# Optimization experiments

Hardware: AMD Instinct MI355X
Metric: run time of the kernel (lower is better)

The kernel has to match this reference:

```python
import jax, jax.numpy as jnp
import numpy as np

CHANNEL = 64
RATIO = 8
C1 = CHANNEL // RATIO


def setup_inputs() -> dict:
    key = jax.random.key(0)
    ks = jax.random.split(key, 8)
    b, c, h, w = 2, CHANNEL, 96, 96
    X = jax.random.normal(ks[0], (b, c, h, w), dtype=jnp.float32)
    Y = jax.random.normal(ks[1], (b, c, h, w), dtype=jnp.float32)
    # 1x1 conv weights (stored as [out, in]) + biases, Kaiming-ish scale
    s = 1.0 / np.sqrt(c)
    Wq = jax.random.uniform(ks[2], (C1, c), jnp.float32, -s, s)
    bq = jax.random.uniform(ks[3], (C1,), jnp.float32, -s, s)
    Wk = jax.random.uniform(ks[4], (C1, c), jnp.float32, -s, s)
    bk = jax.random.uniform(ks[5], (C1,), jnp.float32, -s, s)
    Wv = jax.random.uniform(ks[6], (c, c), jnp.float32, -s, s)
    bv = jax.random.uniform(ks[7], (c,), jnp.float32, -s, s)
    return {"X": X, "Y": Y, "Wq": Wq, "bq": bq, "Wk": Wk, "bk": bk, "Wv": Wv, "bv": bv}


def reference(X, Y, Wq, bq, Wk, bk, Wv, bv):
    b, c, h, w = Y.shape
    n = h * w
    # 1x1 convs as channel contractions -> [b, n, c_out]
    Xf = X.reshape(b, c, n)                       # [b, c, n]
    q = jnp.einsum('oc,bcn->bno', Wq, Xf) + bq    # [b, n, c1]
    k = jnp.einsum('oc,bcn->bno', Wk, Xf) + bk    # [b, n, c1]
    v = jnp.einsum('oc,bcn->bno', Wv, Y.reshape(b, c, n)) + bv  # [b, n, c]
    scores = jnp.einsum('bic,bjc->bij', q, k)     # [b, n, n]
    # NOTE: softmax over dim=1 (the first n axis), as in the original module
    a = jax.nn.softmax(scores, axis=1)
    x = jnp.einsum('bij,bjc->bic', a, v)          # [b, n, c]
    x = x.transpose(0, 2, 1).reshape(b, c, h, w)
    return Y + x
```

## Files before the change

### kernel.cpp

```cpp
#include <hip/hip_runtime.h>

#define NPOS 9216
#define NB 2
#define CCH 64

typedef __attribute__((ext_vector_type(8))) short short8;
typedef __attribute__((ext_vector_type(4))) float f32x4;

__device__ __forceinline__ ushort f2bf(float x) {
    unsigned u = __builtin_bit_cast(unsigned, x);
    u += 0x7FFFu + ((u >> 16) & 1u);
    return (ushort)(u >> 16);
}

__global__ __launch_bounds__(256) void qkv_kernel(
    const float* __restrict__ X, const float* __restrict__ Y,
    const float* __restrict__ Wq, const float* __restrict__ bq,
    const float* __restrict__ Wk, const float* __restrict__ bk,
    const float* __restrict__ Wv, const float* __restrict__ bv,
    ushort* __restrict__ qb, ushort* __restrict__ kb, float* __restrict__ v)
{
    __shared__ float wqkT[1024];
    __shared__ float wvT[4096];
    int tid = threadIdx.x;
    for (int idx = tid; idx < 1024; idx += 256) {
        int c = idx >> 4, o = idx & 15;
        wqkT[idx] = (o < 8) ? Wq[o * 64 + c] : Wk[(o - 8) * 64 + c];
    }
    for (int idx = tid; idx < 4096; idx += 256) {
        int c = idx >> 6, o = idx & 63;
        wvT[idx] = Wv[o * 64 + c];
    }
    __syncthreads();

    int p = tid & 63, s = tid >> 6;
    int base = blockIdx.x * 64;
    int b = base / NPOS;
    int n = (base % NPOS) + p;

    float va[16], qk[8];
    #pragma unroll
    for (int o = 0; o < 16; ++o) va[o] = bv[s * 16 + o];
    #pragma unroll
    for (int o = 0; o < 8; ++o) qk[o] = 0.f;
    if (s == 0) {
        #pragma unroll
        for (int o = 0; o < 8; ++o) qk[o] = bq[o];
    } else if (s == 1) {
        #pragma unroll
        for (int o = 0; o < 8; ++o) qk[o] = bk[o];
    }

    const float* Xb = X + (size_t)b * CCH * NPOS + n;
    const float* Yb = Y + (size_t)b * CCH * NPOS + n;
    for (int c = 0; c < 64; ++c) {
        float yv = Yb[(size_t)c * NPOS];
        const float4* wv4 = (const float4*)(wvT + c * 64 + s * 16);
        #pragma unroll
        for (int o4 = 0; o4 < 4; ++o4) {
            float4 wv = wv4[o4];
            va[o4*4+0] += wv.x * yv; va[o4*4+1] += wv.y * yv;
            va[o4*4+2] += wv.z * yv; va[o4*4+3] += wv.w * yv;
        }
        if (s < 2) {
            float xv = Xb[(size_t)c * NPOS];
            const float4* wq4 = (const float4*)(wqkT + c * 16 + s * 8);
            float4 w0 = wq4[0], w1 = wq4[1];
            qk[0] += w0.x * xv; qk[1] += w0.y * xv;
            qk[2] += w0.z * xv; qk[3] += w0.w * xv;
            qk[4] += w1.x * xv; qk[5] += w1.y * xv;
            qk[6] += w1.z * xv; qk[7] += w1.w * xv;
        }
    }
    float4* vdst = (float4*)(v + ((size_t)b * NPOS + n) * 64 + s * 16);
    #pragma unroll
    for (int o4 = 0; o4 < 4; ++o4)
        vdst[o4] = make_float4(va[o4*4], va[o4*4+1], va[o4*4+2], va[o4*4+3]);
    if (s < 2) {
        short8 row;
        #pragma unroll
        for (int o = 0; o < 8; ++o) row[o] = (short)f2bf(qk[o]);
        ushort* dst = (s == 0 ? qb : kb) + ((size_t)b * NPOS + n) * 8;
        *(short8*)dst = row;
    }
}

__global__ __launch_bounds__(256) void zpass_kernel(
    const ushort* __restrict__ qb, const ushort* __restrict__ kb,
    float* __restrict__ Z)
{
    int tid = threadIdx.x;
    int w = tid >> 6, l = tid & 63;
    int il = l & 15, g = l >> 4;
    int b = blockIdx.z;
    int jb = blockIdx.x * 64 + w * 16;
    const short8 zero8 = {0,0,0,0,0,0,0,0};
    const f32x4 cz = {0.f,0.f,0.f,0.f};

    short8 kf = zero8;
    if (g == 0) kf = *(const short8*)(kb + ((size_t)b * NPOS + jb + il) * 8);

    float za[4] = {0.f, 0.f, 0.f, 0.f};
    const ushort* qrow = qb + ((size_t)b * NPOS + blockIdx.y * 2304 + il) * 8;
    for (int is = 0; is < 144; ++is) {
        short8 qf = *(const short8*)(qrow + (size_t)is * 128);
        if (g != 0) qf = zero8;
        f32x4 sv = __builtin_amdgcn_mfma_f32_16x16x32_bf16(kf, qf, cz, 0, 0, 0);
        za[0] += __expf(sv[0]);
        za[1] += __expf(sv[1]);
        za[2] += __expf(sv[2]);
        za[3] += __expf(sv[3]);
    }
    #pragma unroll
    for (int r = 0; r < 4; ++r) {
        float x = za[r];
        x += __shfl_xor(x, 1, 16);
        x += __shfl_xor(x, 2, 16);
        x += __shfl_xor(x, 4, 16);
        x += __shfl_xor(x, 8, 16);
        za[r] = x;
    }
    if (il == 0) {
        #pragma unroll
        for (int r = 0; r < 4; ++r)
            atomicAdd(&Z[(size_t)b * NPOS + jb + g * 4 + r], za[r]);
    }
}

__global__ __launch_bounds__(256) void scalevT_kernel(
    const float* __restrict__ v, const float* __restrict__ Z,
    ushort* __restrict__ VzT)
{
    int tid = threadIdx.x;
    int p = tid & 63, s = tid >> 6;
    int base = blockIdx.x * 64;
    int b = base / NPOS;
    int n = (base % NPOS) + p;
    float rz = 1.0f / Z[(size_t)b * NPOS + n];
    const float4* vr = (const float4*)(v + ((size_t)b * NPOS + n) * 64 + s * 16);
    ushort* dst = VzT + (size_t)b * CCH * NPOS + n;
    #pragma unroll
    for (int q4 = 0; q4 < 4; ++q4) {
        float4 a = vr[q4];
        size_t c0 = s * 16 + q4 * 4;
        dst[(c0 + 0) * NPOS] = f2bf(a.x * rz);
        dst[(c0 + 1) * NPOS] = f2bf(a.y * rz);
        dst[(c0 + 2) * NPOS] = f2bf(a.z * rz);
        dst[(c0 + 3) * NPOS] = f2bf(a.w * rz);
    }
}

__global__ __launch_bounds__(256) void pass2_kernel(
    const ushort* __restrict__ qb, const ushort* __restrict__ kb,
    const ushort* __restrict__ VzT, float* __restrict__ out)
{
    __shared__ ushort vz_lds[2][2048];
    __shared__ ushort p_lds[4][512];
    int tid = threadIdx.x;
    int w = tid >> 6, l = tid & 63;
    int il = l & 15, g = l >> 4;
    int b = blockIdx.z;
    int ibase = blockIdx.x * 64 + w * 16;
    int j0 = blockIdx.y * 1152;

    const short8 zero8 = {0,0,0,0,0,0,0,0};
    const f32x4 cz = {0.f,0.f,0.f,0.f};

    short8 qf = zero8;
    if (g == 0) qf = *(const short8*)(qb + ((size_t)b * NPOS + ibase + il) * 8);

    f32x4 acc[4];
    #pragma unroll
    for (int cg = 0; cg < 4; ++cg) acc[cg] = cz;

    const ushort* kbb = kb + (size_t)b * NPOS * 8;
    int sc = tid >> 2, sslot = tid & 3;
    const ushort* vsrc = VzT + (size_t)b * CCH * NPOS + (size_t)sc * NPOS + j0 + sslot * 8;

    *(float4*)&vz_lds[0][sc * 32 + sslot * 8] = *(const float4*)vsrc;
    __syncthreads();

    int swz = (il >> 1) & 3;
    ushort* pw = p_lds[w];

    for (int st = 0; st < 36; ++st) {
        int jb = j0 + st * 32;
        int cur = st & 1;
        bool more = (st + 1) < 36;
        float4 nv = {0.f,0.f,0.f,0.f};
        if (more) nv = *(const float4*)(vsrc + (size_t)(st + 1) * 32);

        short8 kf0 = zero8, kf1 = zero8;
        if (g == 0) {
            kf0 = *(const short8*)(kbb + (size_t)(jb + il) * 8);
            kf1 = *(const short8*)(kbb + (size_t)(jb + 16 + il) * 8);
        }
        f32x4 s0 = __builtin_amdgcn_mfma_f32_16x16x32_bf16(kf0, qf, cz, 0, 0, 0);
        f32x4 s1 = __builtin_amdgcn_mfma_f32_16x16x32_bf16(kf1, qf, cz, 0, 0, 0);

        int rowoff = il * 32 + (g & 1) * 4;
        {
            int stored = ((g >> 1) ^ swz);
            unsigned u01 = (unsigned)f2bf(__expf(s0[0])) | ((unsigned)f2bf(__expf(s0[1])) << 16);
            unsigned u23 = (unsigned)f2bf(__expf(s0[2])) | ((unsigned)f2bf(__expf(s0[3])) << 16);
            *(unsigned*)&pw[rowoff + stored * 8 + 0] = u01;
            *(unsigned*)&pw[rowoff + stored * 8 + 2] = u23;
        }
        {
            int stored = ((2 | (g >> 1)) ^ swz);
            unsigned u01 = (unsigned)f2bf(__expf(s1[0])) | ((unsigned)f2bf(__expf(s1[1])) << 16);
            unsigned u23 = (unsigned)f2bf(__expf(s1[2])) | ((unsigned)f2bf(__expf(s1[3])) << 16);
            *(unsigned*)&pw[rowoff + stored * 8 + 0] = u01;
            *(unsigned*)&pw[rowoff + stored * 8 + 2] = u23;
        }

        short8 pf = *(short8*)&pw[il * 32 + ((g ^ swz) * 8)];

        #pragma unroll
        for (int cg = 0; cg < 4; ++cg) {
            short8 af = *(short8*)&vz_lds[cur][(cg * 16 + il) * 32 + g * 8];
            acc[cg] = __builtin_amdgcn_mfma_f32_16x16x32_bf16(af, pf, acc[cg], 0, 0, 0);
        }

        if (more) *(float4*)&vz_lds[cur ^ 1][sc * 32 + sslot * 8] = nv;
        __syncthreads();
    }

    float* ob = out + (size_t)b * CCH * NPOS + ibase + il;
    #pragma unroll
    for (int cg = 0; cg < 4; ++cg) {
        #pragma unroll
        for (int r = 0; r < 4; ++r) {
            int c = cg * 16 + g * 4 + r;
            atomicAdd(ob + (size_t)c * NPOS, acc[cg][r]);
        }
    }
}

extern "C" void kernel_launch(void* const* d_in, const int* in_sizes, int n_in,
                              void* d_out, int out_size, void* d_ws, size_t ws_size,
                              hipStream_t stream) {
    const float* X  = (const float*)d_in[0];
    const float* Y  = (const float*)d_in[1];
    const float* Wq = (const float*)d_in[2];
    const float* bq = (const float*)d_in[3];
    const float* Wk = (const float*)d_in[4];
    const float* bk = (const float*)d_in[5];
    const float* Wv = (const float*)d_in[6];
    const float* bv = (const float*)d_in[7];

    char* ws = (char*)d_ws;
    ushort* qb  = (ushort*)(ws);
    ushort* kbw = (ushort*)(ws + 294912);
    ushort* VzT = (ushort*)(ws + 589824);
    float*  v   = (float*) (ws + 2949120);
    float*  Z   = (float*) (ws + 7667712);

    hipMemsetAsync(Z, 0, (size_t)NB * NPOS * sizeof(float), stream);

    qkv_kernel<<<288, 256, 0, stream>>>(X, Y, Wq, bq, Wk, bk, Wv, bv, qb, kbw, v);
    zpass_kernel<<<dim3(144, 4, NB), 256, 0, stream>>>(qb, kbw, Z);
    scalevT_kernel<<<288, 256, 0, stream>>>(v, Z, VzT);

    hipMemcpyAsync(d_out, Y, (size_t)NB * CCH * NPOS * sizeof(float),
                   hipMemcpyDeviceToDevice, stream);
    pass2_kernel<<<dim3(144, 8, NB), 256, 0, stream>>>(qb, kbw, VzT, (float*)d_out);
}
```

Before: 205.2 us.

## Fuse residual copy into qkv, use exp2 with folded log2e, pad LDS, fewer splits

Copies Y into the output inside the qkv kernel instead of a separate device memcpy, and prescales q by log2(e) so both softmax passes can use the native exp2. Replaces the software bf16 rounding with the packed hardware convert instruction. Pads the V tile rows in LDS to reduce bank conflicts and halves the j-split of pass2, which halves the output atomics at the cost of less grid parallelism. Rounding q after scaling slightly changes numerics.

```diff
diff --git a/kernel.cpp b/kernel.cpp
--- a/kernel.cpp
+++ b/kernel.cpp
@@ -3,14 +3,23 @@
 #define NPOS 9216
 #define NB 2
 #define CCH 64
+#define VZP 40
 
 typedef __attribute__((ext_vector_type(8))) short short8;
 typedef __attribute__((ext_vector_type(4))) float f32x4;
+
+#define LOG2E 1.4426950408889634f
 
 __device__ __forceinline__ ushort f2bf(float x) {
     unsigned u = __builtin_bit_cast(unsigned, x);
     u += 0x7FFFu + ((u >> 16) & 1u);
     return (ushort)(u >> 16);
+}
+
+__device__ __forceinline__ unsigned cvt_pk_bf16(float lo, float hi) {
+    unsigned r;
+    asm("v_cvt_pk_bf16_f32 %0, %1, %2" : "=v"(r) : "v"(lo), "v"(hi));
+    return r;
 }
 
 __global__ __launch_bounds__(256) void qkv_kernel(
@@ -18,7 +27,8 @@
     const float* __restrict__ Wq, const float* __restrict__ bq,
     const float* __restrict__ Wk, const float* __restrict__ bk,
     const float* __restrict__ Wv, const float* __restrict__ bv,
-    ushort* __restrict__ qb, ushort* __restrict__ kb, float* __restrict__ v)
+    ushort* __restrict__ qb, ushort* __restrict__ kb, float* __restrict__ v,
+    float* __restrict__ out)
 {
     __shared__ float wqkT[1024];
     __shared__ float wvT[4096];
@@ -53,8 +63,10 @@
 
     const float* Xb = X + (size_t)b * CCH * NPOS + n;
     const float* Yb = Y + (size_t)b * CCH * NPOS + n;
+    float* ob = out + (size_t)b * CCH * NPOS + n;
     for (int c = 0; c < 64; ++c) {
         float yv = Yb[(size_t)c * NPOS];
+        ob[(size_t)c * NPOS] = yv;
         const float4* wv4 = (const float4*)(wvT + c * 64 + s * 16);
         #pragma unroll
         for (int o4 = 0; o4 < 4; ++o4) {
@@ -77,6 +89,10 @@
     for (int o4 = 0; o4 < 4; ++o4)
         vdst[o4] = make_float4(va[o4*4], va[o4*4+1], va[o4*4+2], va[o4*4+3]);
     if (s < 2) {
+        if (s == 0) {
+            #pragma unroll
+            for (int o = 0; o < 8; ++o) qk[o] *= LOG2E;
+        }
         short8 row;
         #pragma unroll
         for (int o = 0; o < 8; ++o) row[o] = (short)f2bf(qk[o]);
@@ -106,10 +122,10 @@
         short8 qf = *(const short8*)(qrow + (size_t)is * 128);
         if (g != 0) qf = zero8;
         f32x4 sv = __builtin_amdgcn_mfma_f32_16x16x32_bf16(kf, qf, cz, 0, 0, 0);
-        za[0] += __expf(sv[0]);
-        za[1] += __expf(sv[1]);
-        za[2] += __expf(sv[2]);
-        za[3] += __expf(sv[3]);
+        za[0] += __builtin_amdgcn_exp2f(sv[0]);
+        za[1] += __builtin_amdgcn_exp2f(sv[1]);
+        za[2] += __builtin_amdgcn_exp2f(sv[2]);
+        za[3] += __builtin_amdgcn_exp2f(sv[3]);
     }
     #pragma unroll
     for (int r = 0; r < 4; ++r) {
@@ -154,14 +170,14 @@
     const ushort* __restrict__ qb, const ushort* __restrict__ kb,
     const ushort* __restrict__ VzT, float* __restrict__ out)
 {
-    __shared__ ushort vz_lds[2][2048];
+    __shared__ ushort vz_lds[2][64 * VZP];
     __shared__ ushort p_lds[4][512];
     int tid = threadIdx.x;
     int w = tid >> 6, l = tid & 63;
     int il = l & 15, g = l >> 4;
     int b = blockIdx.z;
     int ibase = blockIdx.x * 64 + w * 16;
-    int j0 = blockIdx.y * 1152;
+    int j0 = blockIdx.y * 2304;
 
     const short8 zero8 = {0,0,0,0,0,0,0,0};
     const f32x4 cz = {0.f,0.f,0.f,0.f};
@@ -177,16 +193,16 @@
     int sc = tid >> 2, sslot = tid & 3;
     const ushort* vsrc = VzT + (size_t)b * CCH * NPOS + (size_t)sc * NPOS + j0 + sslot * 8;
 
-    *(float4*)&vz_lds[0][sc * 32 + sslot * 8] = *(const float4*)vsrc;
+    *(float4*)&vz_lds[0][sc * VZP + sslot * 8] = *(const float4*)vsrc;
     __syncthreads();
 
     int swz = (il >> 1) & 3;
     ushort* pw = p_lds[w];
 
-    for (int st = 0; st < 36; ++st) {
+    for (int st = 0; st < 72; ++st) {
         int jb = j0 + st * 32;
         int cur = st & 1;
-        bool more = (st + 1) < 36;
+        bool more = (st + 1) < 72;
         float4 nv = {0.f,0.f,0.f,0.f};
         if (more) nv = *(const float4*)(vsrc + (size_t)(st + 1) * 32);
 
@@ -201,15 +217,19 @@
         int rowoff = il * 32 + (g & 1) * 4;
         {
             int stored = ((g >> 1) ^ swz);
-            unsigned u01 = (unsigned)f2bf(__expf(s0[0])) | ((unsigned)f2bf(__expf(s0[1])) << 16);
-            unsigned u23 = (unsigned)f2bf(__expf(s0[2])) | ((unsigned)f2bf(__expf(s0[3])) << 16);
+            unsigned u01 = cvt_pk_bf16(__builtin_amdgcn_exp2f(s0[0]),
+                                       __builtin_amdgcn_exp2f(s0[1]));
+            unsigned u23 = cvt_pk_bf16(__builtin_amdgcn_exp2f(s0[2]),
+                                       __builtin_amdgcn_exp2f(s0[3]));
             *(unsigned*)&pw[rowoff + stored * 8 + 0] = u01;
             *(unsigned*)&pw[rowoff + stored * 8 + 2] = u23;
         }
         {
             int stored = ((2 | (g >> 1)) ^ swz);
-            unsigned u01 = (unsigned)f2bf(__expf(s1[0])) | ((unsigned)f2bf(__expf(s1[1])) << 16);
-            unsigned u23 = (unsigned)f2bf(__expf(s1[2])) | ((unsigned)f2bf(__expf(s1[3])) << 16);
+            unsigned u01 = cvt_pk_bf16(__builtin_amdgcn_exp2f(s1[0]),
+                                       __builtin_amdgcn_exp2f(s1[1]));
+            unsigned u23 = cvt_pk_bf16(__builtin_amdgcn_exp2f(s1[2]),
+                                       __builtin_amdgcn_exp2f(s1[3]));
             *(unsigned*)&pw[rowoff + stored * 8 + 0] = u01;
             *(unsigned*)&pw[rowoff + stored * 8 + 2] = u23;
         }
@@ -218,11 +238,11 @@
 
         #pragma unroll
         for (int cg = 0; cg < 4; ++cg) {
-            short8 af = *(short8*)&vz_lds[cur][(cg * 16 + il) * 32 + g * 8];
+            short8 af = *(short8*)&vz_lds[cur][(cg * 16 + il) * VZP + g * 8];
             acc[cg] = __builtin_amdgcn_mfma_f32_16x16x32_bf16(af, pf, acc[cg], 0, 0, 0);
         }
 
-        if (more) *(float4*)&vz_lds[cur ^ 1][sc * 32 + sslot * 8] = nv;
+        if (more) *(float4*)&vz_lds[cur ^ 1][sc * VZP + sslot * 8] = nv;
         __syncthreads();
     }
 
@@ -258,11 +278,9 @@
 
     hipMemsetAsync(Z, 0, (size_t)NB * NPOS * sizeof(float), stream);
 
-    qkv_kernel<<<288, 256, 0, stream>>>(X, Y, Wq, bq, Wk, bk, Wv, bv, qb, kbw, v);
+    qkv_kernel<<<288, 256, 0, stream>>>(X, Y, Wq, bq, Wk, bk, Wv, bv,
+                                        qb, kbw, v, (float*)d_out);
     zpass_kernel<<<dim3(144, 4, NB), 256, 0, stream>>>(qb, kbw, Z);
     scalevT_kernel<<<288, 256, 0, stream>>>(v, Z, VzT);
-
-    hipMemcpyAsync(d_out, Y, (size_t)NB * CCH * NPOS * sizeof(float),
-                   hipMemcpyDeviceToDevice, stream);
-    pass2_kernel<<<dim3(144, 8, NB), 256, 0, stream>>>(qb, kbw, VzT, (float*)d_out);
-}
+    pass2_kernel<<<dim3(144, 4, NB), 256, 0, stream>>>(qb, kbw, VzT, (float*)d_out);
+}
```

After: 207.6 us. No clear change (+1.2%).
